# Kernel tuning notes

Measured on AMD Instinct MI355X. Metric: run time of the kernel, lower is better.

Reference implementation:

```python
import jax, jax.numpy as jnp
import numpy as np
import math

N_NODES = 50000
M = 200000          # number of (node, hyperedge) incidences
NE = 20000          # number of hyperedges (= hyperedge_index[1].max()+1)
NI = 8              # num_inds (inducing points)
DIN = 64            # dim_in
DV = 64             # dim_out == dim_V
NH = 4              # num_heads
DH = DV // NH


def setup_inputs() -> dict:
    key = jax.random.key(0)
    ks = jax.random.split(key, 24)
    node_idx = jax.random.randint(ks[0], (M,), 0, N_NODES, dtype=jnp.int32)
    edge_idx = jax.random.randint(ks[1], (M,), 0, NE, dtype=jnp.int32)
    # guarantee num_edges == NE (matches num_edges = max+1 in torch code)
    edge_idx = edge_idx.at[-1].set(NE - 1)
    hyperedge_index = jnp.stack([node_idx, edge_idx], axis=0)

    def lin(k, fan_in, shape):
        return jax.random.normal(k, shape, dtype=jnp.float32) / np.sqrt(fan_in)

    inp = {
        "X": jax.random.normal(ks[2], (N_NODES, DIN), dtype=jnp.float32),
        "hyperedge_index": hyperedge_index,
        "I": lin(ks[3], DV, (NI, DV)),  # xavier-ish inducing points
    }
    names = ["m0_wq", "m0_bq", "m0_wk", "m0_bk", "m0_wv", "m0_bv", "m0_wo", "m0_bo",
             "m1_wq", "m1_bq", "m1_wk", "m1_bk", "m1_wv", "m1_bv", "m1_wo", "m1_bo"]
    for i, n in enumerate(names):
        k = ks[4 + i]
        if n.endswith("b" + n[-1]) and n[3] == 'b':
            inp[n] = lin(k, DV, (DV,))
        else:
            inp[n] = lin(k, DV, (DV, DV))
    return inp


def _segment_softmax(a, seg, num_segments):
    # a: [E, NH]; segment-wise stable softmax along E grouped by seg
    amax = jax.ops.segment_max(a, seg, num_segments=num_segments)
    amax = jnp.where(jnp.isfinite(amax), amax, jnp.zeros_like(amax))
    e = jnp.exp(a - amax[seg])
    den = jax.ops.segment_sum(e, seg, num_segments=num_segments)
    return e / den[seg]


def _mab(Qin, Kin, wq, bq, wk, bk, wv, bv, wo, bo,
         q_idx, k_idx, seg, out_idx, num_segments):
    Q = Qin @ wq + bq            # [Nq, DV]
    K = Kin @ wk + bk            # [Nk, DV]
    V = Kin @ wv + bv            # [Nk, DV]
    # gather per extended edge, split into heads: [E, NH, DH]
    Qi = Q[q_idx].reshape(-1, NH, DH)
    Kj = K[k_idx].reshape(-1, NH, DH)
    Vj = V[k_idx].reshape(-1, NH, DH)
    A = (Qi * Kj).sum(-1) / math.sqrt(DV)               # [E, NH]
    A = _segment_softmax(A, seg, num_segments)           # segment softmax over LE_index
    QKV = jax.ops.segment_sum(A[..., None] * Vj, seg, num_segments=num_segments)  # [ns, NH, DH]
    O = Q[out_idx].reshape(-1, NH, DH) + QKV              # [ns, NH, DH]
    # torch: stack heads at dim0 then permute(1,2,0).reshape -> [N, DH, NH] flatten
    O = jnp.transpose(O, (0, 2, 1)).reshape(-1, DV)
    return O + jax.nn.relu(O @ wo + bo)


def reference(X, hyperedge_index, I,
              m0_wq, m0_bq, m0_wk, m0_bk, m0_wv, m0_bv, m0_wo, m0_bo,
              m1_wq, m1_bq, m1_wk, m1_bk, m1_wv, m1_bv, m1_wo, m1_bo):
    node = hyperedge_index[0]                 # [M]
    edge = hyperedge_index[1]                 # [M]
    node_t = jnp.tile(node, NI)               # [M*NI]
    edge_t = jnp.tile(edge, NI)
    inc = jnp.repeat(jnp.arange(NI, dtype=edge.dtype), M)
    ext2 = edge_t * NI + inc                  # index into I_big rows / segments for mab0

    I_big = jnp.tile(I, (NE, 1))              # [NE*NI, DV]
    # mab0: queries = inducing points (per edge), keys/values = X
    H = _mab(I_big, X,
             m0_wq, m0_bq, m0_wk, m0_bk, m0_wv, m0_bv, m0_wo, m0_bo,
             q_idx=ext2, k_idx=node_t, seg=ext2,
             out_idx=jnp.arange(NE * NI), num_segments=NE * NI)

    seg1 = jnp.tile(jnp.arange(M, dtype=edge.dtype), NI)
    # mab1: queries = X, keys/values = H; output one row per incidence
    O = _mab(X, H,
             m1_wq, m1_bq, m1_wk, m1_bk, m1_wv, m1_bv, m1_wo, m1_bo,
             q_idx=node_t, k_idx=ext2, seg=seg1,
             out_idx=node, num_segments=M)
    return O  # [M, DV]; original returns (O, None)
```

## Files before the change

kernel.cpp:

```cpp
#include <hip/hip_runtime.h>
#include <math.h>

#define NNODES 50000
#define MINC   200000
#define NEDGE  20000
#define NIND   8

#define SCALE_LOG2E 0.18033688f

typedef __attribute__((ext_vector_type(8))) short bf16x8;
typedef __attribute__((ext_vector_type(4))) float f32x4;

__device__ __forceinline__ short f2bf(float f) {
    union { float f; unsigned u; } x; x.f = f;
    unsigned r = x.u + 0x7FFF + ((x.u >> 16) & 1);
    return (short)(r >> 16);
}
__device__ __forceinline__ float bf2f(short s) {
    union { unsigned u; float f; } x; x.u = ((unsigned)(unsigned short)s) << 16;
    return x.f;
}
__device__ __forceinline__ int qperm(int c) { return ((c & 15) << 2) | (c >> 4); }
__device__ __forceinline__ int sigperm(int c) { return ((c & 3) << 4) | (c >> 2); }

__global__ void setup_hist_kernel(const float* __restrict__ I,
                                  const float* __restrict__ m0_wq, const float* __restrict__ m0_bq,
                                  const float* __restrict__ m0_wk, const float* __restrict__ m0_bk,
                                  const float* __restrict__ m0_wv, const float* __restrict__ m0_bv,
                                  const float* __restrict__ m1_wq, const float* __restrict__ m1_bq,
                                  const float* __restrict__ m0_wo, const float* __restrict__ m1_wk,
                                  const float* __restrict__ m1_wv, const float* __restrict__ m1_wo,
                                  float* __restrict__ QI, float* __restrict__ bias160,
                                  short* __restrict__ Wt0, short* __restrict__ WtO,
                                  short* __restrict__ WtK, short* __restrict__ WtV,
                                  short* __restrict__ WtF,
                                  const int* __restrict__ edge, int* __restrict__ cnt) {
    __shared__ float QIs[512];
    __shared__ float Wf[2048];
    __shared__ float bfS[32];
    int tid = threadIdx.x, bid = blockIdx.x;
    if (bid >= 6) {
        int m = (bid - 6) * 512 + tid;
        if (m < MINC) atomicAdd(&cnt[edge[m]], 1);
        return;
    }
    {
        int i = tid >> 6, c = tid & 63;
        float acc = m0_bq[c];
        for (int k = 0; k < 64; ++k) acc += I[i * 64 + k] * m0_wq[k * 64 + c];
        QIs[tid] = acc;
    }
    __syncthreads();
    if (bid == 0) {
        QI[tid] = QIs[tid];
        if (tid < 32) {
            int i = tid >> 2, h = tid & 3;
            float s = 0.f;
            for (int d = 0; d < 16; ++d)
                s += m0_bk[h * 16 + d] * QIs[i * 64 + h * 16 + d];
            bfS[tid] = s * SCALE_LOG2E;
        }
        __syncthreads();
        if (tid < 160)
            bias160[tid] = (tid < 64) ? m0_bv[tid]
                         : ((tid < 96) ? bfS[tid - 64] : m1_bq[tid - 96]);
    } else if (bid == 1) {
        for (int idx = tid; idx < 2048; idx += 512) {
            int k = idx >> 5, j = idx & 31;
            int i = j >> 2, h = j & 3;
            float s = 0.f;
            for (int d = 0; d < 16; ++d)
                s += m0_wk[k * 64 + h * 16 + d] * QIs[i * 64 + h * 16 + d];
            Wf[idx] = s * SCALE_LOG2E;
        }
        __syncthreads();
        for (int idx = tid; idx < 160 * 72; idx += 512) {
            int c = idx / 72, k = idx % 72;
            short v = 0;
            if (k < 64) {
                float f = (c < 64) ? m0_wv[k * 64 + c]
                        : (c < 96) ? Wf[k * 32 + (c - 64)]
                                   : m1_wq[k * 64 + (c - 96)];
                v = f2bf(f);
            }
            Wt0[idx] = v;
        }
    } else {
        int mat = bid - 2;
        const float* W = (mat == 0) ? m0_wo : (mat == 1) ? m1_wk : (mat == 2) ? m1_wv : m1_wo;
        short* D = (mat == 0) ? WtO : (mat == 1) ? WtK : (mat == 2) ? WtV : WtF;
        bool cperm = (mat == 0);
        for (int idx = tid; idx < 64 * 72; idx += 512) {
            int c = idx / 72, k = idx % 72;
            short v = 0;
            if (k < 64) {
                int kk = qperm(k);
                int cc = cperm ? qperm(c) : c;
                v = f2bf(W[kk * 64 + cc]);
            }
            D[idx] = v;
        }
    }
}

#define NALLOCB ((NEDGE + 255) / 256)
__global__ void gemmx_alloc_kernel(const float* __restrict__ A,
                                   const short* __restrict__ Wt, const float* __restrict__ bias,
                                   short* __restrict__ V0, _Float16* __restrict__ S0,
                                   short* __restrict__ Q1,
                                   const int* __restrict__ cnt, int2* __restrict__ rowcnt,
                                   int* __restrict__ cursor, int* __restrict__ total) {
    __shared__ short As[64 * 72];
    __shared__ short Ws[160 * 72];
    int tid = threadIdx.x;
    if (blockIdx.x < NALLOCB) {
        int e = blockIdx.x * 256 + tid;
        int lane = tid & 63;
        int c = (e < NEDGE) ? cnt[e] : 0;
        int v = c;
        #pragma unroll
        for (int off = 1; off < 64; off <<= 1) {
            int t = __shfl_up(v, off);
            if (lane >= off) v += t;
        }
        int wavesum = __shfl(v, 63);
        int base = 0;
        if (lane == 63) base = atomicAdd(total, wavesum);
        base = __shfl(base, 63);
        int excl = base + v - c;
        if (e < NEDGE) {
            rowcnt[e] = make_int2(excl, c);
            cursor[e] = excl;
        }
        return;
    }
    int row0 = (blockIdx.x - NALLOCB) * 64;
    {
        const uint4* wsrc = (const uint4*)Wt;
        uint4* wdst = (uint4*)Ws;
        for (int k = tid; k < 1440; k += 256) wdst[k] = wsrc[k];
    }
    {
        int r = tid >> 2, c0 = (tid & 3) * 16;
        int gr = row0 + r;
        float f[16];
        if (gr < NNODES) {
            const float4* src = (const float4*)(A + (size_t)gr * 64 + c0);
            #pragma unroll
            for (int j = 0; j < 4; ++j) {
                float4 t4 = src[j];
                f[4*j] = t4.x; f[4*j+1] = t4.y; f[4*j+2] = t4.z; f[4*j+3] = t4.w;
            }
        } else {
            #pragma unroll
            for (int j = 0; j < 16; ++j) f[j] = 0.f;
        }
        short tmp[16];
        #pragma unroll
        for (int j = 0; j < 16; ++j) tmp[j] = f2bf(f[j]);
        uint4* dst = (uint4*)&As[r * 72 + c0];
        dst[0] = *(const uint4*)&tmp[0];
        dst[1] = *(const uint4*)&tmp[8];
    }
    __syncthreads();
    int w = tid >> 6, l = tid & 63;
    int lr16 = l & 15, lk = (l >> 4) * 8;
    f32x4 acc[10] = {};
    #pragma unroll
    for (int ks = 0; ks < 2; ++ks) {
        bf16x8 a = *(const bf16x8*)&As[(w * 16 + lr16) * 72 + ks * 32 + lk];
        #pragma unroll
        for (int t = 0; t < 10; ++t) {
            bf16x8 b = *(const bf16x8*)&Ws[(t * 16 + lr16) * 72 + ks * 32 + lk];
            acc[t] = __builtin_amdgcn_mfma_f32_16x16x32_bf16(a, b, acc[t], 0, 0, 0);
        }
    }
    int rbase = w * 16 + (l >> 4) * 4;
    #pragma unroll
    for (int t = 0; t < 10; ++t) {
        int c = t * 16 + lr16;
        float bb = bias[c];
        #pragma unroll
        for (int r = 0; r < 4; ++r) {
            int gr = row0 + rbase + r;
            if (gr < NNODES) {
                float val = acc[t][r] + bb;
                if (c < 64) V0[(size_t)gr * 64 + c] = f2bf(val);
                else if (c < 96) S0[(size_t)gr * 32 + (c - 64)] = (_Float16)val;
                else Q1[(size_t)gr * 64 + (c - 96)] = f2bf(val);
            }
        }
    }
}

__global__ void scatter_kernel(const int* __restrict__ node, const int* __restrict__ edge,
                               int* __restrict__ cursor, int2* __restrict__ csr_nm) {
    int m = blockIdx.x * 256 + threadIdx.x;
    if (m < MINC) {
        int e = edge[m];
        int pos = atomicAdd(&cursor[e], 1);
        csr_nm[pos] = make_int2(node[m], m);
    }
}

__global__ void fused_hkv_mfma_kernel(const short* __restrict__ Opre0,
                                      const short* __restrict__ WtO, const float* __restrict__ bo,
                                      const short* __restrict__ WtK, const float* __restrict__ bk,
                                      const short* __restrict__ WtV, const float* __restrict__ bv,
                                      short* __restrict__ K1, short* __restrict__ V1) {
    __shared__ short As[64 * 72];
    __shared__ short Wo[64 * 72];
    __shared__ short Wk[64 * 72];
    __shared__ short Wv[64 * 72];
    int tid = threadIdx.x;
    int row0 = blockIdx.x * 64;
    {
        uint4* d0 = (uint4*)Wo; const uint4* s0 = (const uint4*)WtO;
        uint4* d1 = (uint4*)Wk; const uint4* s1 = (const uint4*)WtK;
        uint4* d2 = (uint4*)Wv; const uint4* s2 = (const uint4*)WtV;
        for (int k = tid; k < 576; k += 256) { d0[k] = s0[k]; d1[k] = s1[k]; d2[k] = s2[k]; }
    }
    {
        int r = tid >> 2, c0 = (tid & 3) * 16;
        const uint4* src = (const uint4*)(Opre0 + (size_t)(row0 + r) * 64 + c0);
        uint4* dst = (uint4*)&As[r * 72 + c0];
        dst[0] = src[0]; dst[1] = src[1];
    }
    __syncthreads();
    int w = tid >> 6, l = tid & 63;
    int lr16 = l & 15, lk = (l >> 4) * 8;
    int rbase = w * 16 + (l >> 4) * 4;
    {
        f32x4 acc[4] = {};
        #pragma unroll
        for (int ks = 0; ks < 2; ++ks) {
            bf16x8 a = *(const bf16x8*)&As[(w * 16 + lr16) * 72 + ks * 32 + lk];
            #pragma unroll
            for (int t = 0; t < 4; ++t) {
                bf16x8 b = *(const bf16x8*)&Wo[(t * 16 + lr16) * 72 + ks * 32 + lk];
                acc[t] = __builtin_amdgcn_mfma_f32_16x16x32_bf16(a, b, acc[t], 0, 0, 0);
            }
        }
        #pragma unroll
        for (int t = 0; t < 4; ++t) {
            int c = t * 16 + lr16;
            float bb = bo[qperm(c)];
            #pragma unroll
            for (int r = 0; r < 4; ++r) {
                float res = bf2f(As[(rbase + r) * 72 + c]);
                float hv = res + fmaxf(acc[t][r] + bb, 0.f);
                As[(rbase + r) * 72 + c] = f2bf(hv);
            }
        }
    }
    {
        f32x4 ak[4] = {}, av[4] = {};
        #pragma unroll
        for (int ks = 0; ks < 2; ++ks) {
            bf16x8 a = *(const bf16x8*)&As[(w * 16 + lr16) * 72 + ks * 32 + lk];
            #pragma unroll
            for (int t = 0; t < 4; ++t) {
                bf16x8 b1 = *(const bf16x8*)&Wk[(t * 16 + lr16) * 72 + ks * 32 + lk];
                ak[t] = __builtin_amdgcn_mfma_f32_16x16x32_bf16(a, b1, ak[t], 0, 0, 0);
                bf16x8 b2 = *(const bf16x8*)&Wv[(t * 16 + lr16) * 72 + ks * 32 + lk];
                av[t] = __builtin_amdgcn_mfma_f32_16x16x32_bf16(a, b2, av[t], 0, 0, 0);
            }
        }
        #pragma unroll
        for (int t = 0; t < 4; ++t) {
            int c = t * 16 + lr16;
            float bbk = bk[c], bbv = bv[c];
            #pragma unroll
            for (int r = 0; r < 4; ++r) {
                size_t gr = (size_t)(row0 + rbase + r);
                K1[gr * 64 + c] = f2bf((ak[t][r] + bbk) * SCALE_LOG2E);
                V1[gr * 64 + c] = f2bf(av[t][r] + bbv);
            }
        }
    }
}

#define CH0 32
__global__ void attn0_kernel(const short* __restrict__ V0, const _Float16* __restrict__ S0,
                             const float* __restrict__ QI,
                             const int2* __restrict__ rowcnt, const int2* __restrict__ csr_nm,
                             short* __restrict__ Opre0) {
    __shared__ float Sw[4][CH0][32];
    __shared__ float Sc[4][32];
    __shared__ float Li[4][32];
    __shared__ int   Ns[4][CH0];
    int w = threadIdx.x >> 6;
    int lane = threadIdx.x & 63;
    int e = blockIdx.x * 4 + w;
    int2 rc = rowcnt[e];
    int start = rc.x, end = rc.x + rc.y;
    int j = lane & 31;
    int pslot = lane >> 5;
    int tj = ((j & 3) << 3) | (j >> 2);
    int col2 = lane & 31;
    int hh = col2 >> 3;
    float runm = -INFINITY, lrun = 0.f;
    float accL[8] = {}, accH[8] = {};
    for (int c0 = start; c0 < end; c0 += CH0) {
        int cnt = min(CH0, end - c0);
        if (lane < CH0) {
            int idx = c0 + min(lane, cnt - 1);
            Ns[w][lane] = csr_nm[idx].x;
        }
        asm volatile("s_waitcnt lgkmcnt(0)" ::: "memory");
        __builtin_amdgcn_sched_barrier(0);
        float cm = -INFINITY;
        for (int p = pslot; p < cnt; p += 2) {
            int n = Ns[w][p];
            float s = (float)S0[(size_t)n * 32 + j];
            Sw[w][p][tj] = s;
            cm = fmaxf(cm, s);
        }
        cm = fmaxf(cm, __shfl_xor(cm, 32));
        float newm = fmaxf(runm, cm);
        float sc = exp2f(runm - newm);
        runm = newm;
        float lsum = 0.f;
        for (int p = pslot; p < cnt; p += 2) {
            float s = Sw[w][p][tj];
            float w_ = exp2f(s - newm);
            Sw[w][p][tj] = w_;
            lsum += w_;
        }
        lsum += __shfl_xor(lsum, 32);
        lrun = lrun * sc + lsum;
        if (pslot == 0) Sc[w][tj] = sc;
        asm volatile("s_waitcnt lgkmcnt(0)" ::: "memory");
        __builtin_amdgcn_sched_barrier(0);
        float4 sA = *(const float4*)&Sc[w][hh * 8];
        float4 sB = *(const float4*)&Sc[w][hh * 8 + 4];
        accL[0] *= sA.x; accH[0] *= sA.x;
        accL[1] *= sA.y; accH[1] *= sA.y;
        accL[2] *= sA.z; accH[2] *= sA.z;
        accL[3] *= sA.w; accH[3] *= sA.w;
        accL[4] *= sB.x; accH[4] *= sB.x;
        accL[5] *= sB.y; accH[5] *= sB.y;
        accL[6] *= sB.z; accH[6] *= sB.z;
        accL[7] *= sB.w; accH[7] *= sB.w;
        int npair = (cnt + 1) >> 1;
        #pragma unroll 4
        for (int k = 0; k < npair; ++k) {
            int rp = 2 * k + pslot;
            bool vld = rp < cnt;
            int rc2 = vld ? rp : (cnt - 1);
            int n = Ns[w][rc2];
            unsigned vp = *(const unsigned*)&V0[(size_t)n * 64 + col2 * 2];
            float vlo = vld ? __int_as_float(vp << 16) : 0.f;
            float vhi = vld ? __int_as_float(vp & 0xffff0000u) : 0.f;
            float4 wA = *(const float4*)&Sw[w][rc2][hh * 8];
            float4 wB = *(const float4*)&Sw[w][rc2][hh * 8 + 4];
            accL[0] += wA.x * vlo; accH[0] += wA.x * vhi;
            accL[1] += wA.y * vlo; accH[1] += wA.y * vhi;
            accL[2] += wA.z * vlo; accH[2] += wA.z * vhi;
            accL[3] += wA.w * vlo; accH[3] += wA.w * vhi;
            accL[4] += wB.x * vlo; accH[4] += wB.x * vhi;
            accL[5] += wB.y * vlo; accH[5] += wB.y * vhi;
            accL[6] += wB.z * vlo; accH[6] += wB.z * vhi;
            accL[7] += wB.w * vlo; accH[7] += wB.w * vhi;
        }
    }
    if (pslot == 0) Li[w][tj] = lrun;
    asm volatile("s_waitcnt lgkmcnt(0)" ::: "memory");
    __builtin_amdgcn_sched_barrier(0);
    #pragma unroll
    for (int i = 0; i < 8; ++i) {
        accL[i] += __shfl_xor(accL[i], 32);
        accH[i] += __shfl_xor(accH[i], 32);
    }
    float4 lA = *(const float4*)&Li[w][hh * 8];
    float4 lB = *(const float4*)&Li[w][hh * 8 + 4];
    float li[8] = {lA.x, lA.y, lA.z, lA.w, lB.x, lB.y, lB.z, lB.w};
    if (pslot == 0) {
        #pragma unroll
        for (int i = 0; i < 8; ++i) {
            float2 qi2 = *(const float2*)&QI[i * 64 + col2 * 2];
            float inv = (li[i] > 0.f) ? 1.f / li[i] : 0.f;
            float ol = qi2.x + accL[i] * inv;
            float oh = qi2.y + accH[i] * inv;
            unsigned res = ((unsigned)(unsigned short)f2bf(oh) << 16)
                         | (unsigned)(unsigned short)f2bf(ol);
            *(unsigned*)&Opre0[(size_t)(e * NIND + i) * 64 + col2 * 2] = res;
        }
    }
}

__global__ void attn1_kernel(const short* __restrict__ Q1, const short* __restrict__ K1,
                             const short* __restrict__ V1,
                             const int2* __restrict__ rowcnt, const int2* __restrict__ csr_nm,
                             short* __restrict__ Opre1) {
    int w = threadIdx.x >> 6;
    int lane = threadIdx.x & 63;
    int e = blockIdx.x * 4 + w;
    int sl4 = lane & 15;
    int inc = lane >> 4;
    float Kf[8][4], Vf[8][4];
    #pragma unroll
    for (int i = 0; i < 8; ++i) {
        uint2 kp = *(const uint2*)&K1[(size_t)(e * 8 + i) * 64 + sl4 * 4];
        uint2 vp = *(const uint2*)&V1[(size_t)(e * 8 + i) * 64 + sl4 * 4];
        Kf[i][0] = __int_as_float(kp.x << 16);
        Kf[i][1] = __int_as_float(kp.x & 0xffff0000u);
        Kf[i][2] = __int_as_float(kp.y << 16);
        Kf[i][3] = __int_as_float(kp.y & 0xffff0000u);
        Vf[i][0] = __int_as_float(vp.x << 16);
        Vf[i][1] = __int_as_float(vp.x & 0xffff0000u);
        Vf[i][2] = __int_as_float(vp.y << 16);
        Vf[i][3] = __int_as_float(vp.y & 0xffff0000u);
    }
    #pragma unroll
    for (int i = 0; i < 8; ++i) {
        #pragma unroll
        for (int d = 0; d < 4; ++d) {
            asm volatile("" : "+v"(Kf[i][d]), "+v"(Vf[i][d]));
        }
    }
    int2 rc = rowcnt[e];
    int start = rc.x, end = rc.x + rc.y;
    #pragma unroll 4
    for (int p0 = start; p0 < end; p0 += 4) {
        int p = p0 + inc;
        bool valid = (p < end);
        int pc = valid ? p : (end - 1);
        int2 nm = csr_nm[pc];
        uint2 qp = *(const uint2*)&Q1[(size_t)nm.x * 64 + sl4 * 4];
        float qa0 = __int_as_float(qp.x << 16);
        float qa1 = __int_as_float(qp.x & 0xffff0000u);
        float qa2 = __int_as_float(qp.y << 16);
        float qa3 = __int_as_float(qp.y & 0xffff0000u);
        float a[8];
        #pragma unroll
        for (int i = 0; i < 8; ++i) {
            float t = qa0 * Kf[i][0] + qa1 * Kf[i][1] + qa2 * Kf[i][2] + qa3 * Kf[i][3];
            int tv = __builtin_amdgcn_update_dpp(0, __float_as_int(t), 0xB1, 0xf, 0xf, true);
            t += __int_as_float(tv);
            tv = __builtin_amdgcn_update_dpp(0, __float_as_int(t), 0x4E, 0xf, 0xf, true);
            t += __int_as_float(tv);
            a[i] = t;
        }
        float mx = fmaxf(fmaxf(fmaxf(a[0], a[1]), fmaxf(a[2], a[3])),
                         fmaxf(fmaxf(a[4], a[5]), fmaxf(a[6], a[7])));
        float l = 0.f, ac0 = 0.f, ac1 = 0.f, ac2 = 0.f, ac3 = 0.f;
        #pragma unroll
        for (int i = 0; i < 8; ++i) {
            float w_ = exp2f(a[i] - mx);
            l += w_;
            ac0 += w_ * Vf[i][0];
            ac1 += w_ * Vf[i][1];
            ac2 += w_ * Vf[i][2];
            ac3 += w_ * Vf[i][3];
        }
        float rl = 1.f / l;
        float o0 = qa0 + ac0 * rl;
        float o1 = qa1 + ac1 * rl;
        float o2 = qa2 + ac2 * rl;
        float o3 = qa3 + ac3 * rl;
        uint2 res;
        res.x = ((unsigned)(unsigned short)f2bf(o1) << 16) | (unsigned)(unsigned short)f2bf(o0);
        res.y = ((unsigned)(unsigned short)f2bf(o3) << 16) | (unsigned)(unsigned short)f2bf(o2);
        if (valid) *(uint2*)&Opre1[(size_t)nm.y * 64 + sl4 * 4] = res;
    }
}

__global__ void gemm_out_kernel(const short* __restrict__ Av,
                                const short* __restrict__ Wt, const float* __restrict__ bias,
                                float* __restrict__ out) {
    __shared__ short As[128 * 72];
    __shared__ short Ws[64 * 72];
    int tid = threadIdx.x;
    int row0 = blockIdx.x * 128;
    {
        const uint4* wsrc = (const uint4*)Wt;
        uint4* wdst = (uint4*)Ws;
        for (int k = tid; k < 576; k += 256) wdst[k] = wsrc[k];
    }
    #pragma unroll
    for (int it = 0; it < 2; ++it) {
        int slot = tid + it * 256;
        int r = slot >> 2, c0 = (slot & 3) * 16;
        int gr = row0 + r;
        uint4 a0 = {}, a1 = {};
        if (gr < MINC) {
            const uint4* src = (const uint4*)(Av + (size_t)gr * 64 + c0);
            a0 = src[0]; a1 = src[1];
        }
        uint4* dst = (uint4*)&As[r * 72 + c0];
        dst[0] = a0; dst[1] = a1;
    }
    __syncthreads();
    int w = tid >> 6, l = tid & 63;
    int lr16 = l & 15, lk = (l >> 4) * 8;
    f32x4 acc[2][4] = {};
    #pragma unroll
    for (int ks = 0; ks < 2; ++ks) {
        bf16x8 a0 = *(const bf16x8*)&As[(w * 16 + lr16) * 72 + ks * 32 + lk];
        bf16x8 a1 = *(const bf16x8*)&As[(64 + w * 16 + lr16) * 72 + ks * 32 + lk];
        #pragma unroll
        for (int t = 0; t < 4; ++t) {
            bf16x8 b = *(const bf16x8*)&Ws[(t * 16 + lr16) * 72 + ks * 32 + lk];
            acc[0][t] = __builtin_amdgcn_mfma_f32_16x16x32_bf16(a0, b, acc[0][t], 0, 0, 0);
            acc[1][t] = __builtin_amdgcn_mfma_f32_16x16x32_bf16(a1, b, acc[1][t], 0, 0, 0);
        }
    }
    int rbase = w * 16 + (l >> 4) * 4;
    #pragma unroll
    for (int rt = 0; rt < 2; ++rt) {
        #pragma unroll
        for (int t = 0; t < 4; ++t) {
            int c = t * 16 + lr16;
            float bb = bias[c];
            int sc = sigperm(c);
            #pragma unroll
            for (int r = 0; r < 4; ++r) {
                int gr = row0 + rt * 64 + rbase + r;
                if (gr < MINC) {
                    float val = acc[rt][t][r] + bb;
                    float res = bf2f(As[(rt * 64 + rbase + r) * 72 + sc]);
                    __builtin_nontemporal_store(res + fmaxf(val, 0.f),
                                                &out[(size_t)gr * 64 + c]);
                }
            }
        }
    }
}

extern "C" void kernel_launch(void* const* d_in, const int* in_sizes, int n_in,
                              void* d_out, int out_size, void* d_ws, size_t ws_size,
                              hipStream_t stream) {
    const float* X    = (const float*)d_in[0];
    const int*   hei  = (const int*)d_in[1];
    const float* I    = (const float*)d_in[2];
    const float* m0_wq = (const float*)d_in[3];
    const float* m0_bq = (const float*)d_in[4];
    const float* m0_wk = (const float*)d_in[5];
    const float* m0_bk = (const float*)d_in[6];
    const float* m0_wv = (const float*)d_in[7];
    const float* m0_bv = (const float*)d_in[8];
    const float* m0_wo = (const float*)d_in[9];
    const float* m0_bo = (const float*)d_in[10];
    const float* m1_wq = (const float*)d_in[11];
    const float* m1_bq = (const float*)d_in[12];
    const float* m1_wk = (const float*)d_in[13];
    const float* m1_bk = (const float*)d_in[14];
    const float* m1_wv = (const float*)d_in[15];
    const float* m1_bv = (const float*)d_in[16];
    const float* m1_wo = (const float*)d_in[17];
    const float* m1_bo = (const float*)d_in[18];

    const int* node = hei;
    const int* edge = hei + MINC;
    float* out = (float*)d_out;

    char* B = (char*)d_ws;
    short* Opre0 = (short*)B;
    short* Opre1 = (short*)B;
    short* V0    = (short*)(B + 20480000);
    _Float16* S0 = (_Float16*)(B + 26880000);
    short* K1    = (short*)(B + 33280000);
    short* V1    = (short*)(B + 53760000);
    short* Q1    = (short*)(B + 74240000);
    float* QI    = (float*)(B + 80640000);
    float* bias160 = QI + 512;
    short* PK    = (short*)(bias160 + 160);
    short* Wt0   = PK;
    short* WtO   = PK + 11520;
    short* WtK   = WtO + 4608;
    short* WtV   = WtK + 4608;
    short* WtF   = WtV + 4608;
    int*   ib       = (int*)(((size_t)(WtF + 4608) + 7) & ~(size_t)7);
    int2*  rowcnt   = (int2*)ib;
    int*   cnt      = (int*)(rowcnt + NEDGE);
    int*   total    = cnt + NEDGE;
    int*   cursor   = total + 1;
    int2*  csr_nm   = (int2*)(((size_t)(cursor + NEDGE) + 7) & ~(size_t)7);

    hipMemsetAsync(cnt, 0, (NEDGE + 1) * sizeof(int), stream);
    setup_hist_kernel<<<6 + (MINC + 511) / 512, 512, 0, stream>>>(
        I, m0_wq, m0_bq, m0_wk, m0_bk, m0_wv, m0_bv,
        m1_wq, m1_bq, m0_wo, m1_wk, m1_wv, m1_wo,
        QI, bias160, Wt0, WtO, WtK, WtV, WtF, edge, cnt);
    gemmx_alloc_kernel<<<NALLOCB + (NNODES + 63) / 64, 256, 0, stream>>>(
        X, Wt0, bias160, V0, S0, Q1, cnt, rowcnt, cursor, total);
    scatter_kernel<<<(MINC + 255) / 256, 256, 0, stream>>>(node, edge, cursor, csr_nm);

    attn0_kernel<<<NEDGE / 4, 256, 0, stream>>>(V0, S0, QI, rowcnt, csr_nm, Opre0);

    fused_hkv_mfma_kernel<<<NEDGE * NIND / 64, 256, 0, stream>>>(
        Opre0, WtO, m0_bo, WtK, m1_bk, WtV, m1_bv, K1, V1);
    attn1_kernel<<<NEDGE / 4, 256, 0, stream>>>(
        Q1, K1, V1, rowcnt, csr_nm, Opre1);
    gemm_out_kernel<<<(MINC + 127) / 128, 256, 0, stream>>>(Opre1, WtF, m1_bo, out);
}
```

Baseline: 158.5 us.

## Fuse H/K/V projection GEMM into attn1 kernel, keeping K1/V1 in LDS

Merges the MFMA kernel that builds H and projects it to K1/V1 with the second attention kernel. Each block of 64 rows (8 hyperedges) now keeps K and V in shared memory and runs attention over those edges' incidences, so the K1/V1 round trip through global memory and one launch go away. Opre1 moves to a separate buffer because Opre0 is still being read. The cost is higher LDS use per block (five 64x72 tiles), fewer blocks, and each wave handling two edges one after the other, which may lower occupancy and load balance.

```diff
diff --git a/kernel.cpp b/kernel.cpp
--- a/kernel.cpp
+++ b/kernel.cpp
@@ -200,83 +200,6 @@
         int e = edge[m];
         int pos = atomicAdd(&cursor[e], 1);
         csr_nm[pos] = make_int2(node[m], m);
-    }
-}
-
-__global__ void fused_hkv_mfma_kernel(const short* __restrict__ Opre0,
-                                      const short* __restrict__ WtO, const float* __restrict__ bo,
-                                      const short* __restrict__ WtK, const float* __restrict__ bk,
-                                      const short* __restrict__ WtV, const float* __restrict__ bv,
-                                      short* __restrict__ K1, short* __restrict__ V1) {
-    __shared__ short As[64 * 72];
-    __shared__ short Wo[64 * 72];
-    __shared__ short Wk[64 * 72];
-    __shared__ short Wv[64 * 72];
-    int tid = threadIdx.x;
-    int row0 = blockIdx.x * 64;
-    {
-        uint4* d0 = (uint4*)Wo; const uint4* s0 = (const uint4*)WtO;
-        uint4* d1 = (uint4*)Wk; const uint4* s1 = (const uint4*)WtK;
-        uint4* d2 = (uint4*)Wv; const uint4* s2 = (const uint4*)WtV;
-        for (int k = tid; k < 576; k += 256) { d0[k] = s0[k]; d1[k] = s1[k]; d2[k] = s2[k]; }
-    }
-    {
-        int r = tid >> 2, c0 = (tid & 3) * 16;
-        const uint4* src = (const uint4*)(Opre0 + (size_t)(row0 + r) * 64 + c0);
-        uint4* dst = (uint4*)&As[r * 72 + c0];
-        dst[0] = src[0]; dst[1] = src[1];
-    }
-    __syncthreads();
-    int w = tid >> 6, l = tid & 63;
-    int lr16 = l & 15, lk = (l >> 4) * 8;
-    int rbase = w * 16 + (l >> 4) * 4;
-    {
-        f32x4 acc[4] = {};
-        #pragma unroll
-        for (int ks = 0; ks < 2; ++ks) {
-            bf16x8 a = *(const bf16x8*)&As[(w * 16 + lr16) * 72 + ks * 32 + lk];
-            #pragma unroll
-            for (int t = 0; t < 4; ++t) {
-                bf16x8 b = *(const bf16x8*)&Wo[(t * 16 + lr16) * 72 + ks * 32 + lk];
-                acc[t] = __builtin_amdgcn_mfma_f32_16x16x32_bf16(a, b, acc[t], 0, 0, 0);
-            }
-        }
-        #pragma unroll
-        for (int t = 0; t < 4; ++t) {
-            int c = t * 16 + lr16;
-            float bb = bo[qperm(c)];
-            #pragma unroll
-            for (int r = 0; r < 4; ++r) {
-                float res = bf2f(As[(rbase + r) * 72 + c]);
-                float hv = res + fmaxf(acc[t][r] + bb, 0.f);
-                As[(rbase + r) * 72 + c] = f2bf(hv);
-            }
-        }
-    }
-    {
-        f32x4 ak[4] = {}, av[4] = {};
-        #pragma unroll
-        for (int ks = 0; ks < 2; ++ks) {
-            bf16x8 a = *(const bf16x8*)&As[(w * 16 + lr16) * 72 + ks * 32 + lk];
-            #pragma unroll
-            for (int t = 0; t < 4; ++t) {
-                bf16x8 b1 = *(const bf16x8*)&Wk[(t * 16 + lr16) * 72 + ks * 32 + lk];
-                ak[t] = __builtin_amdgcn_mfma_f32_16x16x32_bf16(a, b1, ak[t], 0, 0, 0);
-                bf16x8 b2 = *(const bf16x8*)&Wv[(t * 16 + lr16) * 72 + ks * 32 + lk];
-                av[t] = __builtin_amdgcn_mfma_f32_16x16x32_bf16(a, b2, av[t], 0, 0, 0);
-            }
-        }
-        #pragma unroll
-        for (int t = 0; t < 4; ++t) {
-            int c = t * 16 + lr16;
-            float bbk = bk[c], bbv = bv[c];
-            #pragma unroll
-            for (int r = 0; r < 4; ++r) {
-                size_t gr = (size_t)(row0 + rbase + r);
-                K1[gr * 64 + c] = f2bf((ak[t][r] + bbk) * SCALE_LOG2E);
-                V1[gr * 64 + c] = f2bf(av[t][r] + bbv);
-            }
-        }
     }
 }
 
@@ -389,80 +312,157 @@
     }
 }
 
-__global__ void attn1_kernel(const short* __restrict__ Q1, const short* __restrict__ K1,
-                             const short* __restrict__ V1,
-                             const int2* __restrict__ rowcnt, const int2* __restrict__ csr_nm,
-                             short* __restrict__ Opre1) {
-    int w = threadIdx.x >> 6;
-    int lane = threadIdx.x & 63;
-    int e = blockIdx.x * 4 + w;
+__global__ void fused_hkv_attn1_kernel(const short* __restrict__ Opre0,
+                                       const short* __restrict__ WtO, const float* __restrict__ bo,
+                                       const short* __restrict__ WtK, const float* __restrict__ bk,
+                                       const short* __restrict__ WtV, const float* __restrict__ bv,
+                                       const short* __restrict__ Q1,
+                                       const int2* __restrict__ rowcnt,
+                                       const int2* __restrict__ csr_nm,
+                                       short* __restrict__ Opre1) {
+    __shared__ short As[64 * 72];
+    __shared__ short Vls[64 * 72];
+    __shared__ short Wo[64 * 72];
+    __shared__ short Wk[64 * 72];
+    __shared__ short Wv[64 * 72];
+    int tid = threadIdx.x;
+    int row0 = blockIdx.x * 64;
+    {
+        uint4* d0 = (uint4*)Wo; const uint4* s0 = (const uint4*)WtO;
+        uint4* d1 = (uint4*)Wk; const uint4* s1 = (const uint4*)WtK;
+        uint4* d2 = (uint4*)Wv; const uint4* s2 = (const uint4*)WtV;
+        for (int k = tid; k < 576; k += 256) { d0[k] = s0[k]; d1[k] = s1[k]; d2[k] = s2[k]; }
+    }
+    {
+        int r = tid >> 2, c0 = (tid & 3) * 16;
+        const uint4* src = (const uint4*)(Opre0 + (size_t)(row0 + r) * 64 + c0);
+        uint4* dst = (uint4*)&As[r * 72 + c0];
+        dst[0] = src[0]; dst[1] = src[1];
+    }
+    __syncthreads();
+    int w = tid >> 6, lane = tid & 63;
+    int lr16 = lane & 15, lk = (lane >> 4) * 8;
+    int rbase = w * 16 + (lane >> 4) * 4;
+    {
+        f32x4 acc[4] = {};
+        #pragma unroll
+        for (int ks = 0; ks < 2; ++ks) {
+            bf16x8 a = *(const bf16x8*)&As[(w * 16 + lr16) * 72 + ks * 32 + lk];
+            #pragma unroll
+            for (int t = 0; t < 4; ++t) {
+                bf16x8 b = *(const bf16x8*)&Wo[(t * 16 + lr16) * 72 + ks * 32 + lk];
+                acc[t] = __builtin_amdgcn_mfma_f32_16x16x32_bf16(a, b, acc[t], 0, 0, 0);
+            }
+        }
+        #pragma unroll
+        for (int t = 0; t < 4; ++t) {
+            int c = t * 16 + lr16;
+            float bb = bo[qperm(c)];
+            #pragma unroll
+            for (int r = 0; r < 4; ++r) {
+                float res = bf2f(As[(rbase + r) * 72 + c]);
+                float hv = res + fmaxf(acc[t][r] + bb, 0.f);
+                As[(rbase + r) * 72 + c] = f2bf(hv);
+            }
+        }
+    }
+    {
+        f32x4 ak[4] = {}, av[4] = {};
+        #pragma unroll
+        for (int ks = 0; ks < 2; ++ks) {
+            bf16x8 a = *(const bf16x8*)&As[(w * 16 + lr16) * 72 + ks * 32 + lk];
+            #pragma unroll
+            for (int t = 0; t < 4; ++t) {
+                bf16x8 b1 = *(const bf16x8*)&Wk[(t * 16 + lr16) * 72 + ks * 32 + lk];
+                ak[t] = __builtin_amdgcn_mfma_f32_16x16x32_bf16(a, b1, ak[t], 0, 0, 0);
+                bf16x8 b2 = *(const bf16x8*)&Wv[(t * 16 + lr16) * 72 + ks * 32 + lk];
+                av[t] = __builtin_amdgcn_mfma_f32_16x16x32_bf16(a, b2, av[t], 0, 0, 0);
+            }
+        }
+        #pragma unroll
+        for (int t = 0; t < 4; ++t) {
+            int c = t * 16 + lr16;
+            float bbk = bk[c], bbv = bv[c];
+            #pragma unroll
+            for (int r = 0; r < 4; ++r) {
+                int rr = rbase + r;
+                As[rr * 72 + c]  = f2bf((ak[t][r] + bbk) * SCALE_LOG2E);
+                Vls[rr * 72 + c] = f2bf(av[t][r] + bbv);
+            }
+        }
+    }
     int sl4 = lane & 15;
     int inc = lane >> 4;
-    float Kf[8][4], Vf[8][4];
-    #pragma unroll
-    for (int i = 0; i < 8; ++i) {
-        uint2 kp = *(const uint2*)&K1[(size_t)(e * 8 + i) * 64 + sl4 * 4];
-        uint2 vp = *(const uint2*)&V1[(size_t)(e * 8 + i) * 64 + sl4 * 4];
-        Kf[i][0] = __int_as_float(kp.x << 16);
-        Kf[i][1] = __int_as_float(kp.x & 0xffff0000u);
-        Kf[i][2] = __int_as_float(kp.y << 16);
-        Kf[i][3] = __int_as_float(kp.y & 0xffff0000u);
-        Vf[i][0] = __int_as_float(vp.x << 16);
-        Vf[i][1] = __int_as_float(vp.x & 0xffff0000u);
-        Vf[i][2] = __int_as_float(vp.y << 16);
-        Vf[i][3] = __int_as_float(vp.y & 0xffff0000u);
-    }
-    #pragma unroll
-    for (int i = 0; i < 8; ++i) {
-        #pragma unroll
-        for (int d = 0; d < 4; ++d) {
-            asm volatile("" : "+v"(Kf[i][d]), "+v"(Vf[i][d]));
-        }
-    }
-    int2 rc = rowcnt[e];
-    int start = rc.x, end = rc.x + rc.y;
-    #pragma unroll 4
-    for (int p0 = start; p0 < end; p0 += 4) {
-        int p = p0 + inc;
-        bool valid = (p < end);
-        int pc = valid ? p : (end - 1);
-        int2 nm = csr_nm[pc];
-        uint2 qp = *(const uint2*)&Q1[(size_t)nm.x * 64 + sl4 * 4];
-        float qa0 = __int_as_float(qp.x << 16);
-        float qa1 = __int_as_float(qp.x & 0xffff0000u);
-        float qa2 = __int_as_float(qp.y << 16);
-        float qa3 = __int_as_float(qp.y & 0xffff0000u);
-        float a[8];
+    for (int le = 0; le < 2; ++le) {
+        int eloc = w * 2 + le;
+        int e = blockIdx.x * 8 + eloc;
+        int lr0 = eloc * 8;
+        float Kf[8][4], Vf[8][4];
         #pragma unroll
         for (int i = 0; i < 8; ++i) {
-            float t = qa0 * Kf[i][0] + qa1 * Kf[i][1] + qa2 * Kf[i][2] + qa3 * Kf[i][3];
-            int tv = __builtin_amdgcn_update_dpp(0, __float_as_int(t), 0xB1, 0xf, 0xf, true);
-            t += __int_as_float(tv);
-            tv = __builtin_amdgcn_update_dpp(0, __float_as_int(t), 0x4E, 0xf, 0xf, true);
-            t += __int_as_float(tv);
-            a[i] = t;
-        }
-        float mx = fmaxf(fmaxf(fmaxf(a[0], a[1]), fmaxf(a[2], a[3])),
-                         fmaxf(fmaxf(a[4], a[5]), fmaxf(a[6], a[7])));
-        float l = 0.f, ac0 = 0.f, ac1 = 0.f, ac2 = 0.f, ac3 = 0.f;
+            uint2 kp = *(const uint2*)&As[(lr0 + i) * 72 + sl4 * 4];
+            uint2 vp = *(const uint2*)&Vls[(lr0 + i) * 72 + sl4 * 4];
+            Kf[i][0] = __int_as_float(kp.x << 16);
+            Kf[i][1] = __int_as_float(kp.x & 0xffff0000u);
+            Kf[i][2] = __int_as_float(kp.y << 16);
+            Kf[i][3] = __int_as_float(kp.y & 0xffff0000u);
+            Vf[i][0] = __int_as_float(vp.x << 16);
+            Vf[i][1] = __int_as_float(vp.x & 0xffff0000u);
+            Vf[i][2] = __int_as_float(vp.y << 16);
+            Vf[i][3] = __int_as_float(vp.y & 0xffff0000u);
+        }
         #pragma unroll
         for (int i = 0; i < 8; ++i) {
-            float w_ = exp2f(a[i] - mx);
-            l += w_;
-            ac0 += w_ * Vf[i][0];
-            ac1 += w_ * Vf[i][1];
-            ac2 += w_ * Vf[i][2];
-            ac3 += w_ * Vf[i][3];
-        }
-        float rl = 1.f / l;
-        float o0 = qa0 + ac0 * rl;
-        float o1 = qa1 + ac1 * rl;
-        float o2 = qa2 + ac2 * rl;
-        float o3 = qa3 + ac3 * rl;
-        uint2 res;
-        res.x = ((unsigned)(unsigned short)f2bf(o1) << 16) | (unsigned)(unsigned short)f2bf(o0);
-        res.y = ((unsigned)(unsigned short)f2bf(o3) << 16) | (unsigned)(unsigned short)f2bf(o2);
-        if (valid) *(uint2*)&Opre1[(size_t)nm.y * 64 + sl4 * 4] = res;
+            #pragma unroll
+            for (int d = 0; d < 4; ++d) {
+                asm volatile("" : "+v"(Kf[i][d]), "+v"(Vf[i][d]));
+            }
+        }
+        int2 rc = rowcnt[e];
+        int start = rc.x, end = rc.x + rc.y;
+        #pragma unroll 4
+        for (int p0 = start; p0 < end; p0 += 4) {
+            int p = p0 + inc;
+            bool valid = (p < end);
+            int pc = valid ? p : (end - 1);
+            int2 nm = csr_nm[pc];
+            uint2 qp = *(const uint2*)&Q1[(size_t)nm.x * 64 + sl4 * 4];
+            float qa0 = __int_as_float(qp.x << 16);
+            float qa1 = __int_as_float(qp.x & 0xffff0000u);
+            float qa2 = __int_as_float(qp.y << 16);
+            float qa3 = __int_as_float(qp.y & 0xffff0000u);
+            float a[8];
+            #pragma unroll
+            for (int i = 0; i < 8; ++i) {
+                float t = qa0 * Kf[i][0] + qa1 * Kf[i][1] + qa2 * Kf[i][2] + qa3 * Kf[i][3];
+                int tv = __builtin_amdgcn_update_dpp(0, __float_as_int(t), 0xB1, 0xf, 0xf, true);
+                t += __int_as_float(tv);
+                tv = __builtin_amdgcn_update_dpp(0, __float_as_int(t), 0x4E, 0xf, 0xf, true);
+                t += __int_as_float(tv);
+                a[i] = t;
+            }
+            float mx = fmaxf(fmaxf(fmaxf(a[0], a[1]), fmaxf(a[2], a[3])),
+                             fmaxf(fmaxf(a[4], a[5]), fmaxf(a[6], a[7])));
+            float l = 0.f, ac0 = 0.f, ac1 = 0.f, ac2 = 0.f, ac3 = 0.f;
+            #pragma unroll
+            for (int i = 0; i < 8; ++i) {
+                float w_ = exp2f(a[i] - mx);
+                l += w_;
+                ac0 += w_ * Vf[i][0];
+                ac1 += w_ * Vf[i][1];
+                ac2 += w_ * Vf[i][2];
+                ac3 += w_ * Vf[i][3];
+            }
+            float rl = 1.f / l;
+            float o0 = qa0 + ac0 * rl;
+            float o1 = qa1 + ac1 * rl;
+            float o2 = qa2 + ac2 * rl;
+            float o3 = qa3 + ac3 * rl;
+            uint2 res;
+            res.x = ((unsigned)(unsigned short)f2bf(o1) << 16) | (unsigned)(unsigned short)f2bf(o0);
+            res.y = ((unsigned)(unsigned short)f2bf(o3) << 16) | (unsigned)(unsigned short)f2bf(o2);
+            if (valid) *(uint2*)&Opre1[(size_t)nm.y * 64 + sl4 * 4] = res;
+        }
     }
 }
 
@@ -557,11 +557,9 @@
 
     char* B = (char*)d_ws;
     short* Opre0 = (short*)B;
-    short* Opre1 = (short*)B;
     short* V0    = (short*)(B + 20480000);
     _Float16* S0 = (_Float16*)(B + 26880000);
-    short* K1    = (short*)(B + 33280000);
-    short* V1    = (short*)(B + 53760000);
+    short* Opre1 = (short*)(B + 33280000);
     short* Q1    = (short*)(B + 74240000);
     float* QI    = (float*)(B + 80640000);
     float* bias160 = QI + 512;
@@ -589,9 +587,7 @@
 
     attn0_kernel<<<NEDGE / 4, 256, 0, stream>>>(V0, S0, QI, rowcnt, csr_nm, Opre0);
 
-    fused_hkv_mfma_kernel<<<NEDGE * NIND / 64, 256, 0, stream>>>(
-        Opre0, WtO, m0_bo, WtK, m1_bk, WtV, m1_bv, K1, V1);
-    attn1_kernel<<<NEDGE / 4, 256, 0, stream>>>(
-        Q1, K1, V1, rowcnt, csr_nm, Opre1);
+    fused_hkv_attn1_kernel<<<NEDGE / 8, 256, 0, stream>>>(
+        Opre0, WtO, m0_bo, WtK, m1_bk, WtV, m1_bv, Q1, rowcnt, csr_nm, Opre1);
     gemm_out_kernel<<<(MINC + 127) / 128, 256, 0, stream>>>(Opre1, WtF, m1_bo, out);
 }
```

Measured after the change: 152.8 us. 3.6% less time.
